# Kernel optimization log

Hardware: AMD Instinct MI355X
Metric: run time of the kernel (lower is better)

The kernel has to match this reference:

```python
import jax, jax.numpy as jnp
import numpy as np

VOCAB = 20
HID = 128
ACT = 3
IN_DIM = VOCAB + 3
NUM_GRAPHS = 64
N_P, E_P = 100000, 1600000
N_M, E_M = 50000, 800000


def _gcn_conv(x, src, dst, W, b, n_nodes):
    deg = jax.ops.segment_sum(jnp.ones(src.shape[0], x.dtype), dst, num_segments=n_nodes) + 1.0
    dinv = jax.lax.rsqrt(deg)
    xw = x @ W                                    # [N, out]
    coef = dinv[src] * dinv[dst]                  # [E]
    agg = jax.ops.segment_sum(xw[src] * coef[:, None], dst, num_segments=n_nodes)
    # self-loop contribution: norm = dinv[i]*dinv[i] = 1/deg[i]
    return agg + xw / deg[:, None] + b


def _mean_pool(x, batch, n_graphs):
    s = jax.ops.segment_sum(x, batch, num_segments=n_graphs)
    cnt = jax.ops.segment_sum(jnp.ones(x.shape[0], x.dtype), batch, num_segments=n_graphs)
    return s / jnp.maximum(cnt, 1.0)[:, None]


def setup_inputs() -> dict:
    key = jax.random.key(0)
    ks = jax.random.split(key, 24)
    d = {}
    d['residue_p'] = jax.random.randint(ks[0], (N_P,), 0, VOCAB)
    d['pos_p'] = jax.random.normal(ks[1], (N_P, 3), jnp.float32)
    d['edge_index_p'] = jax.random.randint(ks[2], (2, E_P), 0, N_P)
    d['batch_p'] = jnp.sort(jax.random.randint(ks[3], (N_P,), 0, NUM_GRAPHS))
    d['residue_m'] = jax.random.randint(ks[4], (N_M,), 0, VOCAB)
    d['pos_m'] = jax.random.normal(ks[5], (N_M, 3), jnp.float32)
    d['edge_index_m'] = jax.random.randint(ks[6], (2, E_M), 0, N_M)
    d['batch_m'] = jnp.sort(jax.random.randint(ks[7], (N_M,), 0, NUM_GRAPHS))
    s = 0.05
    d['W_p1'] = jax.random.normal(ks[8], (IN_DIM, HID), jnp.float32) * s
    d['b_p1'] = jnp.zeros((HID,), jnp.float32)
    d['W_p2'] = jax.random.normal(ks[9], (HID, HID), jnp.float32) * s
    d['b_p2'] = jnp.zeros((HID,), jnp.float32)
    d['W_m1'] = jax.random.normal(ks[10], (IN_DIM, HID), jnp.float32) * s
    d['b_m1'] = jnp.zeros((HID,), jnp.float32)
    d['W_m2'] = jax.random.normal(ks[11], (HID, HID), jnp.float32) * s
    d['b_m2'] = jnp.zeros((HID,), jnp.float32)
    d['W1'] = jax.random.normal(ks[12], (2 * HID, HID), jnp.float32) * s
    d['b1'] = jnp.zeros((HID,), jnp.float32)
    d['W2'] = jax.random.normal(ks[13], (HID, ACT), jnp.float32) * s
    d['b2'] = jnp.zeros((ACT,), jnp.float32)
    return d


def reference(residue_p, pos_p, edge_index_p, batch_p,
              residue_m, pos_m, edge_index_m, batch_m,
              W_p1, b_p1, W_p2, b_p2, W_m1, b_m1, W_m2, b_m2,
              W1, b1, W2, b2):
    # protein branch
    x_p = jnp.concatenate([jax.nn.one_hot(residue_p, VOCAB, dtype=jnp.float32), pos_p], axis=1)
    sp, dp = edge_index_p[0], edge_index_p[1]
    x_p = jax.nn.relu(_gcn_conv(x_p, sp, dp, W_p1, b_p1, N_P))
    x_p = jax.nn.relu(_gcn_conv(x_p, sp, dp, W_p2, b_p2, N_P))
    protein_embedding = _mean_pool(x_p, batch_p, NUM_GRAPHS)  # [G, HID]
    # micromolecule branch
    x_m = jnp.concatenate([jax.nn.one_hot(residue_m, VOCAB, dtype=jnp.float32), pos_m], axis=1)
    sm, dm = edge_index_m[0], edge_index_m[1]
    x_m = jax.nn.relu(_gcn_conv(x_m, sm, dm, W_m1, b_m1, N_M))
    x_m = jax.nn.relu(_gcn_conv(x_m, sm, dm, W_m2, b_m2, N_M))
    # inject protein context per micromolecule node
    ctx = protein_embedding[batch_m]                # [N_M, HID]
    feat = jnp.concatenate([x_m, ctx], axis=1)      # [N_M, 2*HID]
    h = jax.nn.relu(feat @ W1 + b1)
    return h @ W2 + b2                              # [N_M, ACT]
```

## Files before the change

kernel.cpp:

```cpp
#include <hip/hip_runtime.h>
#include <hip/hip_bf16.h>
#include <hip/hip_fp16.h>

#define HID 128
#define BIN_T 8192
#define NBMAX 1664
#define CAP 2560

typedef _Float16 f16;
typedef __attribute__((ext_vector_type(2))) _Float16 f16x2;
typedef __attribute__((ext_vector_type(4))) _Float16 f16x4;
typedef __attribute__((ext_vector_type(8))) _Float16 f16x8;
typedef __attribute__((ext_vector_type(4))) float f32x4;



__global__ void k_prep_all(const float* __restrict__ Wp2, const float* __restrict__ Wm2,
                           const float* __restrict__ W1,
                           f16* __restrict__ Wp2t, f16* __restrict__ Wm2t,
                           f16* __restrict__ W1at,
                           int* __restrict__ bcur_p, int* __restrict__ bcur_m,
                           const int* __restrict__ batch_p, int* __restrict__ pcnt,
                           float* __restrict__ psum, int N_P) {
    int idx = blockIdx.x * 256 + threadIdx.x;
    if (idx < 16384) {
        int n = idx & 127, k = idx >> 7;
        Wp2t[n * 128 + k] = (f16)Wp2[k * 128 + n];
        Wm2t[n * 128 + k] = (f16)Wm2[k * 128 + n];
        W1at[n * 128 + k] = (f16)W1[k * 128 + n];
    }
    if (idx <= NBMAX) { bcur_p[idx] = idx * CAP; bcur_m[idx] = idx * CAP; }
    if (idx < 64 * HID) psum[idx] = 0.f;
    if (idx < 64) {
        int g = idx;
        int lo = 0, hi = N_P;
        while (lo < hi) { int mid = (lo + hi) >> 1; if (batch_p[mid] < g) lo = mid + 1; else hi = mid; }
        int a = lo;
        lo = 0; hi = N_P;
        while (lo < hi) { int mid = (lo + hi) >> 1; if (batch_p[mid] < g + 1) lo = mid + 1; else hi = mid; }
        pcnt[g] = lo - a;
    }
}


__global__ void k_tile_bin2(const int* __restrict__ src_p, const int* __restrict__ dst_p,
                            const int* __restrict__ res_p,
                            int* __restrict__ bcur_p, unsigned int* __restrict__ pairs_p,
                            int E_p, int NB_p, int TP,
                            const int* __restrict__ src_m, const int* __restrict__ dst_m,
                            const int* __restrict__ res_m,
                            int* __restrict__ bcur_m, unsigned int* __restrict__ pairs_m,
                            int E_m, int NB_m) {
    __shared__ unsigned int dbuf[BIN_T];
    __shared__ unsigned short perm[BIN_T];
    __shared__ int hist[NBMAX];
    __shared__ int lbase[NBMAX];
    __shared__ int gbase[NBMAX];
    __shared__ int tt[256];
    bool isP = (int)blockIdx.x < TP;
    const int* src = isP ? src_p : src_m;
    const int* dst = isP ? dst_p : dst_m;
    const int* res = isP ? res_p : res_m;
    int* bcursor = isP ? bcur_p : bcur_m;
    unsigned int* pairs = isP ? pairs_p : pairs_m;
    int E = isP ? E_p : E_m;
    int NB = isP ? NB_p : NB_m;
    int tilebase = (isP ? blockIdx.x : blockIdx.x - TP) * BIN_T;
    int t = threadIdx.x;
    int n = min(BIN_T, E - tilebase);
    for (int i = t; i < NB; i += 256) hist[i] = 0;
    __syncthreads();
    for (int i = t; i < n; i += 256) {
        unsigned int d = (unsigned int)dst[tilebase + i];
        dbuf[i] = d;
        atomicAdd(&hist[d >> 6], 1);
    }
    __syncthreads();
    {
        int b0 = t * 7, loc[7], run = 0;
        #pragma unroll
        for (int k = 0; k < 7; ++k) {
            int b = b0 + k;
            int c = (b < NB) ? hist[b] : 0;
            loc[k] = run; run += c;
        }
        tt[t] = run;
        __syncthreads();
        int val = run;
        for (int off = 1; off < 256; off <<= 1) {
            int add = (t >= off) ? tt[t - off] : 0;
            __syncthreads();
            tt[t] += add;
            __syncthreads();
        }
        int ebase = tt[t] - val;
        #pragma unroll
        for (int k = 0; k < 7; ++k) {
            int b = b0 + k;
            if (b < NB) lbase[b] = ebase + loc[k];
        }
    }
    __syncthreads();
    for (int i = t; i < NB; i += 256) {
        int c = hist[i];
        gbase[i] = (c > 0) ? atomicAdd(&bcursor[i], c) : 0;
    }
    __syncthreads();
    for (int i = t; i < NB; i += 256) hist[i] = lbase[i];
    __syncthreads();
    for (int i = t; i < n; i += 256) {
        int b = (int)(dbuf[i] >> 6);
        int p = atomicAdd(&hist[b], 1);
        perm[p] = (unsigned short)i;
    }
    __syncthreads();
    for (int p = t; p < n; p += 256) {
        int li = perm[p];
        unsigned int d = dbuf[li];
        int b = (int)(d >> 6);
        int addr = gbase[b] + (p - lbase[b]);
        int sv = src[tilebase + li];
        pairs[addr] = (unsigned int)sv | ((unsigned int)res[sv] << 17) | ((d & 63u) << 26);
    }
}


__global__ void k_fill_a(
        const unsigned int* __restrict__ pairs_p, const int* __restrict__ bcur_p,
        const float* __restrict__ pos_p, f16x4* __restrict__ rec8_p,
        float* __restrict__ dinv_p, int* __restrict__ rowptr_p, int* __restrict__ rowend_p,
        int N_p, int NB_p,
        const unsigned int* __restrict__ pairs_m, const int* __restrict__ bcur_m,
        const float* __restrict__ pos_m, f16x4* __restrict__ rec8_m,
        float* __restrict__ dinv_m, int* __restrict__ rowptr_m, int* __restrict__ rowend_m,
        int N_m) {
    __shared__ int cnt[64];
    bool isP = (int)blockIdx.x < NB_p;
    const unsigned int* pairs = isP ? pairs_p : pairs_m;
    const int* bcur = isP ? bcur_p : bcur_m;
    const float* pos = isP ? pos_p : pos_m;
    f16x4* rec8 = isP ? rec8_p : rec8_m;
    float* dinvA = isP ? dinv_p : dinv_m;
    int* rowptr = isP ? rowptr_p : rowptr_m;
    int* rowend = isP ? rowend_p : rowend_m;
    int N = isP ? N_p : N_m;
    int b = isP ? blockIdx.x : blockIdx.x - NB_p;
    int t = threadIdx.x, base = b * 64;
    if (t < 64) cnt[t] = 0;
    __syncthreads();
    int lo = b * CAP, hi = bcur[b];
    for (int e = lo + t; e < hi; e += 256)
        atomicAdd(&cnt[pairs[e] >> 26], 1);
    __syncthreads();
    if (t < 64) {
        int off = 0;
        for (int k = 0; k < t; ++k) off += cnt[k];
        int node = base + t;
        if (node < N) {
            rowptr[node] = lo + off;
            rowend[node] = lo + off + cnt[t];
            float d = (float)cnt[t] + 1.0f;
            float di = 1.0f / sqrtf(d);
            dinvA[node] = di;
            float px = pos[node * 3 + 0], py = pos[node * 3 + 1], pz = pos[node * 3 + 2];
            f16x4 r;
            r[0] = (f16)di; r[1] = (f16)(di * px); r[2] = (f16)(di * py); r[3] = (f16)(di * pz);
            rec8[node] = r;
        }
    }
}


__global__ __launch_bounds__(256) void k_l1_csr(
        const unsigned int* __restrict__ pairs_p, const int* __restrict__ bcur_p,
        const f16x4* __restrict__ rec8_p, const int* __restrict__ res_p,
        const int* __restrict__ rowptr_p, int* __restrict__ csr_p,
        const float* __restrict__ W_p, const float* __restrict__ bias_p,
        const float* __restrict__ dinv_p, f16* __restrict__ y1_p, int N_p, int NB_p,
        const unsigned int* __restrict__ pairs_m, const int* __restrict__ bcur_m,
        const f16x4* __restrict__ rec8_m, const int* __restrict__ res_m,
        const int* __restrict__ rowptr_m, int* __restrict__ csr_m,
        const float* __restrict__ W_m, const float* __restrict__ bias_m,
        const float* __restrict__ dinv_m, f16* __restrict__ y1_m, int N_m) {
    __shared__ float acc[64][25];
    __shared__ float sdv[64];
    __shared__ int cur[64];
    bool isP = (int)blockIdx.x < NB_p;
    const unsigned int* pairs = isP ? pairs_p : pairs_m;
    const int* bcur = isP ? bcur_p : bcur_m;
    const f16x4* rec8 = isP ? rec8_p : rec8_m;
    const int* residue = isP ? res_p : res_m;
    const int* rowptr = isP ? rowptr_p : rowptr_m;
    int* csr_src = isP ? csr_p : csr_m;
    const float* W = isP ? W_p : W_m;
    const float* bias = isP ? bias_p : bias_m;
    const float* dinvA = isP ? dinv_p : dinv_m;
    f16* y1h = isP ? y1_p : y1_m;
    int N = isP ? N_p : N_m;
    int b = isP ? blockIdx.x : blockIdx.x - NB_p;
    int t = threadIdx.x, base = b * 64;
    for (int q = t; q < 64 * 25; q += 256) ((float*)acc)[q] = 0.f;
    if (t < 64) {
        int node = base + t;
        if (node < N) { sdv[t] = dinvA[node]; cur[t] = rowptr[node]; }
        else cur[t] = 0;
    }
    int jj = (t & 63) * 2, slot = t >> 6;
    float wreg[23][2];
    #pragma unroll
    for (int k = 0; k < 23; ++k) {
        float2 wv = *(const float2*)&W[k * 128 + jj];
        wreg[k][0] = wv.x; wreg[k][1] = wv.y;
    }
    __syncthreads();
    int lo = b * CAP, hi = bcur[b];
    for (int e = lo + t; e < hi; e += 512) {
        unsigned int pk0 = pairs[e];
        int e1 = e + 256;
        bool h1 = e1 < hi;
        unsigned int pk1 = pairs[h1 ? e1 : e];
        int s0 = (int)(pk0 & 0x1FFFFu), s1 = (int)(pk1 & 0x1FFFFu);
        f16x4 r0 = rec8[s0];
        f16x4 r1 = rec8[s1];
        int dl0 = (int)(pk0 >> 26), rs0 = (int)((pk0 >> 17) & 31u);
        int slot0 = atomicAdd(&cur[dl0], 1);
        csr_src[slot0] = s0;
        atomicAdd(&acc[dl0][rs0], (float)r0[0]);
        atomicAdd(&acc[dl0][20], (float)r0[1]);
        atomicAdd(&acc[dl0][21], (float)r0[2]);
        atomicAdd(&acc[dl0][22], (float)r0[3]);
        if (h1) {
            int dl1 = (int)(pk1 >> 26), rs1 = (int)((pk1 >> 17) & 31u);
            int slot1 = atomicAdd(&cur[dl1], 1);
            csr_src[slot1] = s1;
            atomicAdd(&acc[dl1][rs1], (float)r1[0]);
            atomicAdd(&acc[dl1][20], (float)r1[1]);
            atomicAdd(&acc[dl1][21], (float)r1[2]);
            atomicAdd(&acc[dl1][22], (float)r1[3]);
        }
    }
    __syncthreads();
    if (t < 64) {
        int node = base + t;
        if (node < N) {
            f16x4 r = rec8[node];
            acc[t][residue[node]] += (float)r[0];
            acc[t][20] += (float)r[1];
            acc[t][21] += (float)r[2];
            acc[t][22] += (float)r[3];
            float di = sdv[t];
            #pragma unroll
            for (int k = 0; k < 23; ++k) acc[t][k] *= di;
        }
    }
    __syncthreads();
    float bj0 = bias[jj], bj1 = bias[jj + 1];
    for (int r = slot * 16; r < slot * 16 + 16; ++r) {
        int node = base + r;
        if (node >= N) break;
        float a0 = bj0, a1 = bj1;
        #pragma unroll
        for (int k = 0; k < 23; ++k) {
            float zv = acc[r][k];
            a0 += zv * wreg[k][0];
            a1 += zv * wreg[k][1];
        }
        float dv = sdv[r];
        f16x2 o;
        o[0] = (f16)(fmaxf(a0, 0.f) * dv);
        o[1] = (f16)(fmaxf(a1, 0.f) * dv);
        *(f16x2*)&y1h[(size_t)node * HID + jj] = o;
    }
}


#define AGG16_TO_LDS(zs, y1h, rowptr, rowend, csr_src, dinvA, N)                \
    {                                                                           \
        const __half2* y2 = (const __half2*)y1h;                                \
        for (int i = 0; i < 4; ++i) {                                           \
            int node = tile + w * 4 + i;                                        \
            int cn = min(node, N - 1);                                          \
            int s0 = rowptr[cn], s1 = rowend[cn];                               \
            float ax = 0.f, ay = 0.f;                                           \
            int e = s0;                                                         \
            for (; e + 8 <= s1; e += 8) {                                       \
                float2 v0 = __half22float2(y2[(size_t)csr_src[e] * 64 + lane]);     \
                float2 v1 = __half22float2(y2[(size_t)csr_src[e + 1] * 64 + lane]); \
                float2 v2 = __half22float2(y2[(size_t)csr_src[e + 2] * 64 + lane]); \
                float2 v3 = __half22float2(y2[(size_t)csr_src[e + 3] * 64 + lane]); \
                float2 v4 = __half22float2(y2[(size_t)csr_src[e + 4] * 64 + lane]); \
                float2 v5 = __half22float2(y2[(size_t)csr_src[e + 5] * 64 + lane]); \
                float2 v6 = __half22float2(y2[(size_t)csr_src[e + 6] * 64 + lane]); \
                float2 v7 = __half22float2(y2[(size_t)csr_src[e + 7] * 64 + lane]); \
                ax += (v0.x + v1.x) + (v2.x + v3.x) + (v4.x + v5.x) + (v6.x + v7.x); \
                ay += (v0.y + v1.y) + (v2.y + v3.y) + (v4.y + v5.y) + (v6.y + v7.y); \
            }                                                                   \
            for (; e + 4 <= s1; e += 4) {                                       \
                float2 v0 = __half22float2(y2[(size_t)csr_src[e] * 64 + lane]);     \
                float2 v1 = __half22float2(y2[(size_t)csr_src[e + 1] * 64 + lane]); \
                float2 v2 = __half22float2(y2[(size_t)csr_src[e + 2] * 64 + lane]); \
                float2 v3 = __half22float2(y2[(size_t)csr_src[e + 3] * 64 + lane]); \
                ax += (v0.x + v1.x) + (v2.x + v3.x);                            \
                ay += (v0.y + v1.y) + (v2.y + v3.y);                            \
            }                                                                   \
            for (; e < s1; ++e) {                                               \
                float2 v = __half22float2(y2[(size_t)csr_src[e] * 64 + lane]);  \
                ax += v.x; ay += v.y;                                           \
            }                                                                   \
            float di = dinvA[cn];                                               \
            float2 vs = __half22float2(y2[(size_t)cn * 64 + lane]);             \
            f16x2 o;                                                            \
            o[0] = (f16)((ax + vs.x) * di);                                     \
            o[1] = (f16)((ay + vs.y) * di);                                     \
            *(f16x2*)&zs[w * 4 + i][lane * 2] = o;                              \
        }                                                                       \
    }                                                                           \
    __syncthreads();


__global__ __launch_bounds__(256) void k_agg_combined(
        const f16* __restrict__ y1p, const int* __restrict__ rpp, const int* __restrict__ rep,
        const int* __restrict__ csrp, const float* __restrict__ dvp,
        const f16* __restrict__ Wp2t, const float* __restrict__ bp2,
        const int* __restrict__ batchp, float* __restrict__ psum, int Np, int PB,
        const f16* __restrict__ y1m, const int* __restrict__ rpm, const int* __restrict__ rem,
        const int* __restrict__ csrm, const float* __restrict__ dvm,
        const f16* __restrict__ Wm2t, const float* __restrict__ bm2,
        f16* __restrict__ x2g, int Nm) {
    __shared__ f16 zs[16][136];
    int t = threadIdx.x, lane = t & 63, w = t >> 6;
    int lr = lane & 15, kb = lane >> 4;
    bool isP = (int)blockIdx.x < PB;
    if (isP) {
        const f16* y1h = y1p;
        int N = Np;
        int tile = blockIdx.x * 16;
        AGG16_TO_LDS(zs, y1h, rpp, rep, csrp, dvp, N)
        int g0 = batchp[min(tile, N - 1)];
        bool uni = (tile + 15 < N) && (g0 == batchp[tile + 15]);
        int gr[4]; bool val[4];
        if (!uni) {
            #pragma unroll
            for (int r = 0; r < 4; ++r) {
                int row = tile + kb * 4 + r;
                val[r] = row < N;
                gr[r] = batchp[min(row, N - 1)];
            }
        }
        f16x8 afr[4];
        #pragma unroll
        for (int kc = 0; kc < 4; ++kc)
            afr[kc] = *(const f16x8*)&zs[lr][kc * 32 + kb * 8];
        #pragma unroll
        for (int q = 0; q < 2; ++q) {
            int ct = w * 2 + q;
            f32x4 c4 = {0.f, 0.f, 0.f, 0.f};
            int col = ct * 16 + lr;
            const f16* wp = Wp2t + (size_t)col * HID + kb * 8;
            #pragma unroll
            for (int kc = 0; kc < 4; ++kc) {
                f16x8 bf = *(const f16x8*)(wp + kc * 32);
                c4 = __builtin_amdgcn_mfma_f32_16x16x32_f16(afr[kc], bf, c4, 0, 0, 0);
            }
            float bj = bp2[col];
            if (uni) {
                float ps = 0.f;
                #pragma unroll
                for (int r = 0; r < 4; ++r) ps += fmaxf(c4[r] + bj, 0.f);
                ps += __shfl_xor(ps, 16);
                ps += __shfl_xor(ps, 32);
                if (kb == 0) atomicAdd(&psum[g0 * HID + col], ps);
            } else {
                #pragma unroll
                for (int r = 0; r < 4; ++r)
                    if (val[r]) atomicAdd(&psum[gr[r] * HID + col], fmaxf(c4[r] + bj, 0.f));
            }
        }
    } else {
        const f16* y1h = y1m;
        int N = Nm;
        int tile = (blockIdx.x - PB) * 16;
        AGG16_TO_LDS(zs, y1h, rpm, rem, csrm, dvm, N)
        f16x8 afr[4];
        #pragma unroll
        for (int kc = 0; kc < 4; ++kc)
            afr[kc] = *(const f16x8*)&zs[lr][kc * 32 + kb * 8];
        __syncthreads();
        #pragma unroll
        for (int q = 0; q < 2; ++q) {
            int ct = w * 2 + q;
            f32x4 c4 = {0.f, 0.f, 0.f, 0.f};
            int col = ct * 16 + lr;
            const f16* wp = Wm2t + (size_t)col * HID + kb * 8;
            #pragma unroll
            for (int kc = 0; kc < 4; ++kc) {
                f16x8 bf = *(const f16x8*)(wp + kc * 32);
                c4 = __builtin_amdgcn_mfma_f32_16x16x32_f16(afr[kc], bf, c4, 0, 0, 0);
            }
            float bj = bm2[col];
            #pragma unroll
            for (int r = 0; r < 4; ++r)
                zs[kb * 4 + r][col] = (f16)fmaxf(c4[r] + bj, 0.f);
        }
        __syncthreads();
        int row = t >> 4, c8 = (t & 15) * 8;
        if (tile + row < N)
            *(f16x8*)&x2g[(size_t)(tile + row) * HID + c8] = *(const f16x8*)&zs[row][c8];
    }
}

__global__ void k_ctxw_div(const float* __restrict__ psum, const int* __restrict__ pcnt,
                           const float* __restrict__ W1, const float* __restrict__ b1,
                           float* __restrict__ ctxW) {
    __shared__ float pr[128];
    int g = blockIdx.x, j = threadIdx.x;
    pr[j] = psum[g * HID + j] / fmaxf((float)pcnt[g], 1.f);
    __syncthreads();
    float a = b1[j];
    #pragma unroll 4
    for (int k = 0; k < HID; ++k) a += pr[k] * W1[(HID + k) * HID + j];
    ctxW[g * HID + j] = a;
}

__global__ __launch_bounds__(256) void k_mm_finish(
        const f16* __restrict__ x2g, const int* __restrict__ batch,
        const float* __restrict__ ctxW, const f16* __restrict__ W1at,
        const float* __restrict__ W2, const float* __restrict__ b2,
        float* __restrict__ out, int N) {
    __shared__ float part[4][16][3];
    int tile = blockIdx.x * 16;
    int t = threadIdx.x, lane = t & 63, w = t >> 6;
    int lr = lane & 15, kb = lane >> 4;
    int cr = min(tile + lr, N - 1);
    f16x8 afr[4];
    #pragma unroll
    for (int kc = 0; kc < 4; ++kc)
        afr[kc] = *(const f16x8*)&x2g[(size_t)cr * HID + kc * 32 + kb * 8];
    int gidx[4];
    #pragma unroll
    for (int r = 0; r < 4; ++r)
        gidx[r] = batch[min(tile + kb * 4 + r, N - 1)];
    float po[4][3] = {};
    #pragma unroll
    for (int q = 0; q < 2; ++q) {
        int ct = w * 2 + q;
        f32x4 c4 = {0.f, 0.f, 0.f, 0.f};
        int col = ct * 16 + lr;
        const f16* wp = W1at + (size_t)col * HID + kb * 8;
        #pragma unroll
        for (int kc = 0; kc < 4; ++kc) {
            f16x8 bf = *(const f16x8*)(wp + kc * 32);
            c4 = __builtin_amdgcn_mfma_f32_16x16x32_f16(afr[kc], bf, c4, 0, 0, 0);
        }
        float w0 = W2[col * 3 + 0], w1 = W2[col * 3 + 1], w2 = W2[col * 3 + 2];
        #pragma unroll
        for (int r = 0; r < 4; ++r) {
            float h = fmaxf(c4[r] + ctxW[gidx[r] * HID + col], 0.f);
            po[r][0] += h * w0;
            po[r][1] += h * w1;
            po[r][2] += h * w2;
        }
    }
    #pragma unroll
    for (int m = 1; m < 16; m <<= 1) {
        #pragma unroll
        for (int r = 0; r < 4; ++r) {
            po[r][0] += __shfl_xor(po[r][0], m);
            po[r][1] += __shfl_xor(po[r][1], m);
            po[r][2] += __shfl_xor(po[r][2], m);
        }
    }
    if (lr == 0) {
        #pragma unroll
        for (int r = 0; r < 4; ++r) {
            part[w][kb * 4 + r][0] = po[r][0];
            part[w][kb * 4 + r][1] = po[r][1];
            part[w][kb * 4 + r][2] = po[r][2];
        }
    }
    __syncthreads();
    if (t < 48) {
        int row = t / 3, c = t - row * 3;
        int gr2 = tile + row;
        if (gr2 < N)
            out[(size_t)gr2 * 3 + c] = part[0][row][c] + part[1][row][c] +
                                       part[2][row][c] + part[3][row][c] + b2[c];
    }
}


extern "C" void kernel_launch(void* const* d_in, const int* in_sizes, int n_in,
                              void* d_out, int out_size, void* d_ws, size_t ws_size,
                              hipStream_t stream) {
    const int*   residue_p = (const int*)d_in[0];
    const float* pos_p     = (const float*)d_in[1];
    const int*   ei_p      = (const int*)d_in[2];
    const int*   batch_p   = (const int*)d_in[3];
    const int*   residue_m = (const int*)d_in[4];
    const float* pos_m     = (const float*)d_in[5];
    const int*   ei_m      = (const int*)d_in[6];
    const int*   batch_m   = (const int*)d_in[7];
    const float* W_p1 = (const float*)d_in[8];
    const float* b_p1 = (const float*)d_in[9];
    const float* W_p2 = (const float*)d_in[10];
    const float* b_p2 = (const float*)d_in[11];
    const float* W_m1 = (const float*)d_in[12];
    const float* b_m1 = (const float*)d_in[13];
    const float* W_m2 = (const float*)d_in[14];
    const float* b_m2 = (const float*)d_in[15];
    const float* W1   = (const float*)d_in[16];
    const float* b1   = (const float*)d_in[17];
    const float* W2   = (const float*)d_in[18];
    const float* b2   = (const float*)d_in[19];

    const int N_P = in_sizes[0];
    const int E_P = in_sizes[2] / 2;
    const int N_M = in_sizes[4];
    const int E_M = in_sizes[6] / 2;
    const int G = 64;
    const int NB_P = (N_P + 63) / 64;
    const int NB_M = (N_M + 63) / 64;
    const int PB = (N_P + 15) / 16;
    const int MB = (N_M + 15) / 16;

    char* ws = (char*)d_ws;
    size_t off = 0;
    auto alloc = [&](size_t bytes) {
        char* p = ws + off;
        off += (bytes + 511) & ~size_t(511);
        return p;
    };
    f16*           y1_p   = (f16*)  alloc((size_t)N_P * HID * 2);
    f16*           y1_m   = (f16*)  alloc((size_t)N_M * HID * 2);
    f16*           x2g    = (f16*)  alloc((size_t)N_M * HID * 2);
    f16x4*         rec8_p = (f16x4*)alloc((size_t)N_P * 8);
    f16x4*         rec8_m = (f16x4*)alloc((size_t)N_M * 8);
    float*         dinv_p = (float*)alloc((size_t)N_P * 4);
    float*         dinv_m = (float*)alloc((size_t)N_M * 4);
    int*           rp_p   = (int*)  alloc((size_t)N_P * 4);
    int*           rp_m   = (int*)  alloc((size_t)N_M * 4);
    int*           re_p   = (int*)  alloc((size_t)N_P * 4);
    int*           re_m   = (int*)  alloc((size_t)N_M * 4);
    int*           bcur_p = (int*)  alloc((NBMAX + 1) * 4);
    int*           bcur_m = (int*)  alloc((NBMAX + 1) * 4);
    unsigned int*  prs_p  = (unsigned int*)alloc((size_t)NB_P * CAP * 4);
    unsigned int*  prs_m  = (unsigned int*)alloc((size_t)NB_M * CAP * 4);
    int*           csr_p  = (int*)  alloc((size_t)NB_P * CAP * 4);
    int*           csr_m  = (int*)  alloc((size_t)NB_M * CAP * 4);
    float*         psum   = (float*)alloc((size_t)G * HID * 4);
    int*           pcnt   = (int*)  alloc((size_t)G * 4);
    float*         ctxW   = (float*)alloc((size_t)G * HID * 4);
    f16*           Wp2t   = (f16*)  alloc(128 * 128 * 2);
    f16*           Wm2t   = (f16*)  alloc(128 * 128 * 2);
    f16*           W1at   = (f16*)  alloc(128 * 128 * 2);

    const int TP = (E_P + BIN_T - 1) / BIN_T;
    const int TM = (E_M + BIN_T - 1) / BIN_T;

    k_prep_all<<<64, 256, 0, stream>>>(W_p2, W_m2, W1, Wp2t, Wm2t, W1at,
                                       bcur_p, bcur_m, batch_p, pcnt, psum, N_P);
    k_tile_bin2<<<TP + TM, 256, 0, stream>>>(ei_p, ei_p + E_P, residue_p, bcur_p, prs_p,
                                             E_P, NB_P, TP,
                                             ei_m, ei_m + E_M, residue_m, bcur_m, prs_m,
                                             E_M, NB_M);
    k_fill_a<<<NB_P + NB_M, 256, 0, stream>>>(
        prs_p, bcur_p, pos_p, rec8_p, dinv_p, rp_p, re_p, N_P, NB_P,
        prs_m, bcur_m, pos_m, rec8_m, dinv_m, rp_m, re_m, N_M);
    k_l1_csr<<<NB_P + NB_M, 256, 0, stream>>>(
        prs_p, bcur_p, rec8_p, residue_p, rp_p, csr_p, W_p1, b_p1, dinv_p, y1_p, N_P, NB_P,
        prs_m, bcur_m, rec8_m, residue_m, rp_m, csr_m, W_m1, b_m1, dinv_m, y1_m, N_M);
    k_agg_combined<<<PB + MB, 256, 0, stream>>>(
        y1_p, rp_p, re_p, csr_p, dinv_p, Wp2t, b_p2, batch_p, psum, N_P, PB,
        y1_m, rp_m, re_m, csr_m, dinv_m, Wm2t, b_m2, x2g, N_M);
    k_ctxw_div<<<G, HID, 0, stream>>>(psum, pcnt, W1, b1, ctxW);
    k_mm_finish<<<MB, 256, 0, stream>>>(x2g, batch_m, ctxW, W1at, W2, b2,
                                        (float*)d_out, N_M);
}
```

Measured before the change: 279.8 us.

## Move residue lookup into per-node record and CSR build into fill kernel

Removes the random residue[src] gather from the edge-binning kernel by packing each node's residue into a 16-byte per-node record alongside its scaled position features. The CSR source-list scatter moves from the layer-1 kernel into k_fill_a, which already walks the bucketed pairs. The layer-1 edge loop is unrolled 4-way so more gathers are in flight. The cost is a wider per-node record (16 instead of 8 bytes) for every gathered edge and a second pass over the pairs in k_fill_a.

```diff
diff --git a/kernel.cpp b/kernel.cpp
--- a/kernel.cpp
+++ b/kernel.cpp
@@ -44,11 +44,9 @@
 
 
 __global__ void k_tile_bin2(const int* __restrict__ src_p, const int* __restrict__ dst_p,
-                            const int* __restrict__ res_p,
                             int* __restrict__ bcur_p, unsigned int* __restrict__ pairs_p,
                             int E_p, int NB_p, int TP,
                             const int* __restrict__ src_m, const int* __restrict__ dst_m,
-                            const int* __restrict__ res_m,
                             int* __restrict__ bcur_m, unsigned int* __restrict__ pairs_m,
                             int E_m, int NB_m) {
     __shared__ unsigned int dbuf[BIN_T];
@@ -60,7 +58,6 @@
     bool isP = (int)blockIdx.x < TP;
     const int* src = isP ? src_p : src_m;
     const int* dst = isP ? dst_p : dst_m;
-    const int* res = isP ? res_p : res_m;
     int* bcursor = isP ? bcur_p : bcur_m;
     unsigned int* pairs = isP ? pairs_p : pairs_m;
     int E = isP ? E_p : E_m;
@@ -119,30 +116,34 @@
         unsigned int d = dbuf[li];
         int b = (int)(d >> 6);
         int addr = gbase[b] + (p - lbase[b]);
-        int sv = src[tilebase + li];
-        pairs[addr] = (unsigned int)sv | ((unsigned int)res[sv] << 17) | ((d & 63u) << 26);
+        pairs[addr] = (unsigned int)src[tilebase + li] | ((d & 63u) << 26);
     }
 }
 
 
 __global__ void k_fill_a(
         const unsigned int* __restrict__ pairs_p, const int* __restrict__ bcur_p,
-        const float* __restrict__ pos_p, f16x4* __restrict__ rec8_p,
-        float* __restrict__ dinv_p, int* __restrict__ rowptr_p, int* __restrict__ rowend_p,
+        const int* __restrict__ res_p, const float* __restrict__ pos_p,
+        int4* __restrict__ rec16_p, float* __restrict__ dinv_p,
+        int* __restrict__ rowptr_p, int* __restrict__ rowend_p, int* __restrict__ csr_p,
         int N_p, int NB_p,
         const unsigned int* __restrict__ pairs_m, const int* __restrict__ bcur_m,
-        const float* __restrict__ pos_m, f16x4* __restrict__ rec8_m,
-        float* __restrict__ dinv_m, int* __restrict__ rowptr_m, int* __restrict__ rowend_m,
+        const int* __restrict__ res_m, const float* __restrict__ pos_m,
+        int4* __restrict__ rec16_m, float* __restrict__ dinv_m,
+        int* __restrict__ rowptr_m, int* __restrict__ rowend_m, int* __restrict__ csr_m,
         int N_m) {
     __shared__ int cnt[64];
+    __shared__ int cur[64];
     bool isP = (int)blockIdx.x < NB_p;
     const unsigned int* pairs = isP ? pairs_p : pairs_m;
     const int* bcur = isP ? bcur_p : bcur_m;
+    const int* residue = isP ? res_p : res_m;
     const float* pos = isP ? pos_p : pos_m;
-    f16x4* rec8 = isP ? rec8_p : rec8_m;
+    int4* rec16 = isP ? rec16_p : rec16_m;
     float* dinvA = isP ? dinv_p : dinv_m;
     int* rowptr = isP ? rowptr_p : rowptr_m;
     int* rowend = isP ? rowend_p : rowend_m;
+    int* csr_src = isP ? csr_p : csr_m;
     int N = isP ? N_p : N_m;
     int b = isP ? blockIdx.x : blockIdx.x - NB_p;
     int t = threadIdx.x, base = b * 64;
@@ -165,33 +166,39 @@
             float px = pos[node * 3 + 0], py = pos[node * 3 + 1], pz = pos[node * 3 + 2];
             f16x4 r;
             r[0] = (f16)di; r[1] = (f16)(di * px); r[2] = (f16)(di * py); r[3] = (f16)(di * pz);
-            rec8[node] = r;
-        }
-    }
-}
-
-
-__global__ __launch_bounds__(256) void k_l1_csr(
+            int4 rc;
+            rc.x = ((const int*)&r)[0];
+            rc.y = ((const int*)&r)[1];
+            rc.z = residue[node];
+            rc.w = 0;
+            rec16[node] = rc;
+        }
+        cur[t] = lo + off;
+    }
+    __syncthreads();
+    for (int e = lo + t; e < hi; e += 256) {
+        unsigned int pk = pairs[e];
+        int slot = atomicAdd(&cur[pk >> 26], 1);
+        csr_src[slot] = (int)(pk & 0x1FFFFu);
+    }
+}
+
+
+__global__ __launch_bounds__(256) void k_l1(
         const unsigned int* __restrict__ pairs_p, const int* __restrict__ bcur_p,
-        const f16x4* __restrict__ rec8_p, const int* __restrict__ res_p,
-        const int* __restrict__ rowptr_p, int* __restrict__ csr_p,
+        const int4* __restrict__ rec16_p,
         const float* __restrict__ W_p, const float* __restrict__ bias_p,
         const float* __restrict__ dinv_p, f16* __restrict__ y1_p, int N_p, int NB_p,
         const unsigned int* __restrict__ pairs_m, const int* __restrict__ bcur_m,
-        const f16x4* __restrict__ rec8_m, const int* __restrict__ res_m,
-        const int* __restrict__ rowptr_m, int* __restrict__ csr_m,
+        const int4* __restrict__ rec16_m,
         const float* __restrict__ W_m, const float* __restrict__ bias_m,
         const float* __restrict__ dinv_m, f16* __restrict__ y1_m, int N_m) {
     __shared__ float acc[64][25];
     __shared__ float sdv[64];
-    __shared__ int cur[64];
     bool isP = (int)blockIdx.x < NB_p;
     const unsigned int* pairs = isP ? pairs_p : pairs_m;
     const int* bcur = isP ? bcur_p : bcur_m;
-    const f16x4* rec8 = isP ? rec8_p : rec8_m;
-    const int* residue = isP ? res_p : res_m;
-    const int* rowptr = isP ? rowptr_p : rowptr_m;
-    int* csr_src = isP ? csr_p : csr_m;
+    const int4* rec16 = isP ? rec16_p : rec16_m;
     const float* W = isP ? W_p : W_m;
     const float* bias = isP ? bias_p : bias_m;
     const float* dinvA = isP ? dinv_p : dinv_m;
@@ -200,11 +207,7 @@
     int b = isP ? blockIdx.x : blockIdx.x - NB_p;
     int t = threadIdx.x, base = b * 64;
     for (int q = t; q < 64 * 25; q += 256) ((float*)acc)[q] = 0.f;
-    if (t < 64) {
-        int node = base + t;
-        if (node < N) { sdv[t] = dinvA[node]; cur[t] = rowptr[node]; }
-        else cur[t] = 0;
-    }
+    if (t < 64 && base + t < N) sdv[t] = dinvA[base + t];
     int jj = (t & 63) * 2, slot = t >> 6;
     float wreg[23][2];
     #pragma unroll
@@ -214,40 +217,43 @@
     }
     __syncthreads();
     int lo = b * CAP, hi = bcur[b];
-    for (int e = lo + t; e < hi; e += 512) {
-        unsigned int pk0 = pairs[e];
-        int e1 = e + 256;
-        bool h1 = e1 < hi;
-        unsigned int pk1 = pairs[h1 ? e1 : e];
-        int s0 = (int)(pk0 & 0x1FFFFu), s1 = (int)(pk1 & 0x1FFFFu);
-        f16x4 r0 = rec8[s0];
-        f16x4 r1 = rec8[s1];
-        int dl0 = (int)(pk0 >> 26), rs0 = (int)((pk0 >> 17) & 31u);
-        int slot0 = atomicAdd(&cur[dl0], 1);
-        csr_src[slot0] = s0;
-        atomicAdd(&acc[dl0][rs0], (float)r0[0]);
-        atomicAdd(&acc[dl0][20], (float)r0[1]);
-        atomicAdd(&acc[dl0][21], (float)r0[2]);
-        atomicAdd(&acc[dl0][22], (float)r0[3]);
-        if (h1) {
-            int dl1 = (int)(pk1 >> 26), rs1 = (int)((pk1 >> 17) & 31u);
-            int slot1 = atomicAdd(&cur[dl1], 1);
-            csr_src[slot1] = s1;
-            atomicAdd(&acc[dl1][rs1], (float)r1[0]);
-            atomicAdd(&acc[dl1][20], (float)r1[1]);
-            atomicAdd(&acc[dl1][21], (float)r1[2]);
-            atomicAdd(&acc[dl1][22], (float)r1[3]);
+    for (int e = lo + t; e < hi; e += 1024) {
+        unsigned int pk[4];
+        int4 rc[4];
+        bool hv[4];
+        #pragma unroll
+        for (int u = 0; u < 4; ++u) {
+            int ee = e + u * 256;
+            hv[u] = ee < hi;
+            pk[u] = pairs[hv[u] ? ee : e];
+        }
+        #pragma unroll
+        for (int u = 0; u < 4; ++u)
+            rc[u] = rec16[pk[u] & 0x1FFFFu];
+        #pragma unroll
+        for (int u = 0; u < 4; ++u) {
+            if (!hv[u]) continue;
+            f16x2 lo2 = *(const f16x2*)&rc[u].x;
+            f16x2 hi2 = *(const f16x2*)&rc[u].y;
+            int dl = (int)(pk[u] >> 26);
+            int rs = rc[u].z;
+            atomicAdd(&acc[dl][rs], (float)lo2[0]);
+            atomicAdd(&acc[dl][20], (float)lo2[1]);
+            atomicAdd(&acc[dl][21], (float)hi2[0]);
+            atomicAdd(&acc[dl][22], (float)hi2[1]);
         }
     }
     __syncthreads();
     if (t < 64) {
         int node = base + t;
         if (node < N) {
-            f16x4 r = rec8[node];
-            acc[t][residue[node]] += (float)r[0];
-            acc[t][20] += (float)r[1];
-            acc[t][21] += (float)r[2];
-            acc[t][22] += (float)r[3];
+            int4 rc = rec16[node];
+            f16x2 lo2 = *(const f16x2*)&rc.x;
+            f16x2 hi2 = *(const f16x2*)&rc.y;
+            acc[t][rc.z] += (float)lo2[0];
+            acc[t][20] += (float)lo2[1];
+            acc[t][21] += (float)hi2[0];
+            acc[t][22] += (float)hi2[1];
             float di = sdv[t];
             #pragma unroll
             for (int k = 0; k < 23; ++k) acc[t][k] *= di;
@@ -530,45 +536,43 @@
         off += (bytes + 511) & ~size_t(511);
         return p;
     };
-    f16*           y1_p   = (f16*)  alloc((size_t)N_P * HID * 2);
-    f16*           y1_m   = (f16*)  alloc((size_t)N_M * HID * 2);
-    f16*           x2g    = (f16*)  alloc((size_t)N_M * HID * 2);
-    f16x4*         rec8_p = (f16x4*)alloc((size_t)N_P * 8);
-    f16x4*         rec8_m = (f16x4*)alloc((size_t)N_M * 8);
-    float*         dinv_p = (float*)alloc((size_t)N_P * 4);
-    float*         dinv_m = (float*)alloc((size_t)N_M * 4);
-    int*           rp_p   = (int*)  alloc((size_t)N_P * 4);
-    int*           rp_m   = (int*)  alloc((size_t)N_M * 4);
-    int*           re_p   = (int*)  alloc((size_t)N_P * 4);
-    int*           re_m   = (int*)  alloc((size_t)N_M * 4);
-    int*           bcur_p = (int*)  alloc((NBMAX + 1) * 4);
-    int*           bcur_m = (int*)  alloc((NBMAX + 1) * 4);
-    unsigned int*  prs_p  = (unsigned int*)alloc((size_t)NB_P * CAP * 4);
-    unsigned int*  prs_m  = (unsigned int*)alloc((size_t)NB_M * CAP * 4);
-    int*           csr_p  = (int*)  alloc((size_t)NB_P * CAP * 4);
-    int*           csr_m  = (int*)  alloc((size_t)NB_M * CAP * 4);
-    float*         psum   = (float*)alloc((size_t)G * HID * 4);
-    int*           pcnt   = (int*)  alloc((size_t)G * 4);
-    float*         ctxW   = (float*)alloc((size_t)G * HID * 4);
-    f16*           Wp2t   = (f16*)  alloc(128 * 128 * 2);
-    f16*           Wm2t   = (f16*)  alloc(128 * 128 * 2);
-    f16*           W1at   = (f16*)  alloc(128 * 128 * 2);
+    f16*           y1_p    = (f16*)  alloc((size_t)N_P * HID * 2);
+    f16*           y1_m    = (f16*)  alloc((size_t)N_M * HID * 2);
+    f16*           x2g     = (f16*)  alloc((size_t)N_M * HID * 2);
+    int4*          rec16_p = (int4*) alloc((size_t)N_P * 16);
+    int4*          rec16_m = (int4*) alloc((size_t)N_M * 16);
+    float*         dinv_p  = (float*)alloc((size_t)N_P * 4);
+    float*         dinv_m  = (float*)alloc((size_t)N_M * 4);
+    int*           rp_p    = (int*)  alloc((size_t)N_P * 4);
+    int*           rp_m    = (int*)  alloc((size_t)N_M * 4);
+    int*           re_p    = (int*)  alloc((size_t)N_P * 4);
+    int*           re_m    = (int*)  alloc((size_t)N_M * 4);
+    int*           bcur_p  = (int*)  alloc((NBMAX + 1) * 4);
+    int*           bcur_m  = (int*)  alloc((NBMAX + 1) * 4);
+    unsigned int*  prs_p   = (unsigned int*)alloc((size_t)NB_P * CAP * 4);
+    unsigned int*  prs_m   = (unsigned int*)alloc((size_t)NB_M * CAP * 4);
+    int*           csr_p   = (int*)  alloc((size_t)NB_P * CAP * 4);
+    int*           csr_m   = (int*)  alloc((size_t)NB_M * CAP * 4);
+    float*         psum    = (float*)alloc((size_t)G * HID * 4);
+    int*           pcnt    = (int*)  alloc((size_t)G * 4);
+    float*         ctxW    = (float*)alloc((size_t)G * HID * 4);
+    f16*           Wp2t    = (f16*)  alloc(128 * 128 * 2);
+    f16*           Wm2t    = (f16*)  alloc(128 * 128 * 2);
+    f16*           W1at    = (f16*)  alloc(128 * 128 * 2);
 
     const int TP = (E_P + BIN_T - 1) / BIN_T;
     const int TM = (E_M + BIN_T - 1) / BIN_T;
 
     k_prep_all<<<64, 256, 0, stream>>>(W_p2, W_m2, W1, Wp2t, Wm2t, W1at,
                                        bcur_p, bcur_m, batch_p, pcnt, psum, N_P);
-    k_tile_bin2<<<TP + TM, 256, 0, stream>>>(ei_p, ei_p + E_P, residue_p, bcur_p, prs_p,
-                                             E_P, NB_P, TP,
-                                             ei_m, ei_m + E_M, residue_m, bcur_m, prs_m,
-                                             E_M, NB_M);
+    k_tile_bin2<<<TP + TM, 256, 0, stream>>>(ei_p, ei_p + E_P, bcur_p, prs_p, E_P, NB_P, TP,
+                                             ei_m, ei_m + E_M, bcur_m, prs_m, E_M, NB_M);
     k_fill_a<<<NB_P + NB_M, 256, 0, stream>>>(
-        prs_p, bcur_p, pos_p, rec8_p, dinv_p, rp_p, re_p, N_P, NB_P,
-        prs_m, bcur_m, pos_m, rec8_m, dinv_m, rp_m, re_m, N_M);
-    k_l1_csr<<<NB_P + NB_M, 256, 0, stream>>>(
-        prs_p, bcur_p, rec8_p, residue_p, rp_p, csr_p, W_p1, b_p1, dinv_p, y1_p, N_P, NB_P,
-        prs_m, bcur_m, rec8_m, residue_m, rp_m, csr_m, W_m1, b_m1, dinv_m, y1_m, N_M);
+        prs_p, bcur_p, residue_p, pos_p, rec16_p, dinv_p, rp_p, re_p, csr_p, N_P, NB_P,
+        prs_m, bcur_m, residue_m, pos_m, rec16_m, dinv_m, rp_m, re_m, csr_m, N_M);
+    k_l1<<<NB_P + NB_M, 256, 0, stream>>>(
+        prs_p, bcur_p, rec16_p, W_p1, b_p1, dinv_p, y1_p, N_P, NB_P,
+        prs_m, bcur_m, rec16_m, W_m1, b_m1, dinv_m, y1_m, N_M);
     k_agg_combined<<<PB + MB, 256, 0, stream>>>(
         y1_p, rp_p, re_p, csr_p, dinv_p, Wp2t, b_p2, batch_p, psum, N_P, PB,
         y1_m, rp_m, re_m, csr_m, dinv_m, Wm2t, b_m2, x2g, N_M);
```

Measured after the change: 278.1 us. About the same (-0.6%).
